# Performance work log

Hardware: AMD Instinct MI355X
Metric: run time of the kernel (lower is better)

The kernel has to match this reference:

```python
import jax, jax.numpy as jnp
import numpy as np

B, S, T = 32, 128, 64
V, E, H = 32000, 256, 512


def setup_inputs() -> dict:
    key = jax.random.key(0)
    ks = jax.random.split(key, 32)
    n = jax.random.normal

    def lin(k, fi, fo):
        kw, kb = jax.random.split(k)
        s = 1.0 / np.sqrt(fi)
        return (jax.random.uniform(kw, (fi, fo), jnp.float32, -s, s),
                jax.random.uniform(kb, (fo,), jnp.float32, -s, s))

    W_enc, b_enc = lin(ks[4], 2 * H, H)      # attention.enc_h_in
    W_prev, b_prev = lin(ks[5], H, H)        # attention.prev_s_in
    W_att, b_att = lin(ks[6], H, 1)          # attention.linear
    Wi_g, bi_g = lin(ks[7], E, 2 * H)        # cell.input_weights
    Wh_g, bh_g = lin(ks[8], H, 2 * H)        # cell.hidden_weights
    Wc_g, bc_g = lin(ks[9], 2 * H, 2 * H)    # cell.ctx_weights
    Wi, bi = lin(ks[10], E, H)               # cell.input_in
    Wh, bh = lin(ks[11], H, H)               # cell.hidden_in
    Wc, bc = lin(ks[12], 2 * H, H)           # cell.ctx_in
    W_out, b_out = lin(ks[13], H, V)         # dec2word

    return dict(
        content=n(ks[0], (B, H), jnp.float32),
        sentiment=n(ks[1], (B, H), jnp.float32),
        hiddens=n(ks[2], (B, S, 2 * H), jnp.float32),
        target=jax.random.randint(ks[3], (B, T), 0, V, jnp.int32),
        embed=n(ks[14], (V, E), jnp.float32) * 0.02,
        W_enc=W_enc, b_enc=b_enc, W_prev=W_prev, b_prev=b_prev,
        W_att=W_att, b_att=b_att,
        Wi_g=Wi_g, bi_g=bi_g, Wh_g=Wh_g, bh_g=bh_g, Wc_g=Wc_g, bc_g=bc_g,
        Wi=Wi, bi=bi, Wh=Wh, bh=bh, Wc=Wc, bc=bc,
        W_out=W_out, b_out=b_out,
    )


def reference(content, sentiment, hiddens, target, embed,
              W_enc, b_enc, W_prev, b_prev, W_att, b_att,
              Wi_g, bi_g, Wh_g, bh_g, Wc_g, bc_g,
              Wi, bi, Wh, bh, Wc, bc, W_out, b_out):
    tgt_emb = embed[target]                       # [B, T, E]
    enc_proj = hiddens @ W_enc + b_enc            # [B, S, H], timestep-invariant

    def step(prev_s, x_t):
        # additive attention
        q = prev_s @ W_prev + b_prev              # [B, H]
        h = jnp.tanh(enc_proj + q[:, None, :])    # [B, S, H]
        score = h @ W_att + b_att                 # [B, S, 1]
        alpha = jax.nn.softmax(score, axis=1)     # over source positions
        ctx = jnp.einsum('bsi,bsh->bh', alpha, hiddens)  # [B, 2H]
        # GRU-like cell (original uses only the first gate, as written)
        gates = x_t @ Wi_g + bi_g + prev_s @ Wh_g + bh_g + ctx @ Wc_g + bc_g
        reset_gate, _update_gate = jnp.split(gates, 2, axis=1)
        r = jax.nn.sigmoid(reset_gate)
        s_tilde = jnp.tanh(x_t @ Wi + bi + prev_s @ Wh + bh + ctx @ Wc + bc)
        new_s = (1.0 - r) * prev_s + r * s_tilde
        return new_s, new_s

    _, dec_h = jax.lax.scan(step, content, jnp.swapaxes(tgt_emb, 0, 1))
    dec_h = jnp.swapaxes(dec_h, 0, 1)             # [B, T, H]
    style_logits = sentiment @ W_out + b_out      # [B, V], same every step
    outputs = (dec_h @ W_out + b_out) + 0.5 * style_logits[:, None, :]
    return outputs                                # [B, T, V]
```

## Files before the change

kernel.cpp:

```cpp
#include <hip/hip_runtime.h>
#include <hip/hip_bf16.h>
#include <math.h>

#define NB 32
#define NS 128
#define NT 64
#define NV 32000
#define NE 256
#define NH 512

typedef short s16x8 __attribute__((ext_vector_type(8)));
typedef float f32x4 __attribute__((ext_vector_type(4)));

__device__ __forceinline__ unsigned short f2bf(float x) {
    union { float f; unsigned u; } v; v.f = x;
    unsigned r = v.u + 0x7FFFu + ((v.u >> 16) & 1u);
    return (unsigned short)(r >> 16);
}
__device__ __forceinline__ float bf2f(short h) {
    union { unsigned u; float f; } x;
    x.u = ((unsigned)(unsigned short)h) << 16;
    return x.f;
}

__device__ __forceinline__ void st_pt(unsigned long long* p, unsigned pay, unsigned tag) {
    unsigned long long v = (unsigned long long)pay | ((unsigned long long)tag << 32);
    asm volatile("global_store_dwordx2 %0, %1, off sc0 sc1" :: "v"(p), "v"(v) : "memory");
}
__device__ __forceinline__ void ld8_pt(const unsigned long long* b0, unsigned long long* v) {
    unsigned long long v0, v1, v2, v3, v4, v5, v6, v7;
    asm volatile(
        "global_load_dwordx2 %0, %8, off sc0 sc1\n\t"
        "global_load_dwordx2 %1, %9, off sc0 sc1\n\t"
        "global_load_dwordx2 %2, %10, off sc0 sc1\n\t"
        "global_load_dwordx2 %3, %11, off sc0 sc1\n\t"
        "global_load_dwordx2 %4, %12, off sc0 sc1\n\t"
        "global_load_dwordx2 %5, %13, off sc0 sc1\n\t"
        "global_load_dwordx2 %6, %14, off sc0 sc1\n\t"
        "global_load_dwordx2 %7, %15, off sc0 sc1\n\t"
        "s_waitcnt vmcnt(0)"
        : "=&v"(v0), "=&v"(v1), "=&v"(v2), "=&v"(v3),
          "=&v"(v4), "=&v"(v5), "=&v"(v6), "=&v"(v7)
        : "v"(b0), "v"(b0 + 1024), "v"(b0 + 2048), "v"(b0 + 3072),
          "v"(b0 + 4096), "v"(b0 + 5120), "v"(b0 + 6144), "v"(b0 + 7168)
        : "memory");
    v[0] = v0; v[1] = v1; v[2] = v2; v[3] = v3;
    v[4] = v4; v[5] = v5; v[6] = v6; v[7] = v7;
}
__device__ __forceinline__ void ld3_pt(const unsigned long long* p0,
                                       const unsigned long long* p1,
                                       const unsigned long long* p2,
                                       unsigned long long& a, unsigned long long& b,
                                       unsigned long long& c) {
    asm volatile(
        "global_load_dwordx2 %0, %3, off sc0 sc1\n\t"
        "global_load_dwordx2 %1, %4, off sc0 sc1\n\t"
        "global_load_dwordx2 %2, %5, off sc0 sc1\n\t"
        "s_waitcnt vmcnt(0)"
        : "=&v"(a), "=&v"(b), "=&v"(c)
        : "v"(p0), "v"(p1), "v"(p2)
        : "memory");
}

__global__ void build_wfrag_k(const float* __restrict__ Wp,
                              const float* __restrict__ Whg,
                              const float* __restrict__ Wh,
                              unsigned short* __restrict__ wfrag) {
    int blk = blockIdx.x;
    int lane = threadIdx.x;
    int ct = blk >> 4, kt = blk & 15;
    int c = ct * 16 + (lane & 15);
    int kb = kt * 32 + (lane >> 4) * 8;
    s16x8 v;
#pragma unroll
    for (int j = 0; j < 8; ++j) {
        int k = kb + j;
        float x;
        if (c < 512)       x = Wp[k * 512 + c];
        else if (c < 1024) x = Whg[k * 1024 + (c - 512)];
        else               x = Wh[k * 512 + (c - 1024)];
        v[j] = (short)f2bf(x);
    }
    ((s16x8*)wfrag)[blk * 64 + lane] = v;
}

template<int MODE>
__global__ __launch_bounds__(256, 2) void gemm_mfma(
    const float* __restrict__ Af, const unsigned short* __restrict__ Abf,
    const int* __restrict__ gidx,
    const float* __restrict__ B0, const float* __restrict__ B1, const float* __restrict__ B2,
    const float* __restrict__ e0, const float* __restrict__ e1, const float* __restrict__ e2,
    const float* __restrict__ e3, const float* __restrict__ e4, const float* __restrict__ e5,
    void* __restrict__ O0v, void* __restrict__ O1v, void* __restrict__ O2v)
{
    constexpr int M   = (MODE == 0) ? 4096 : 2048;
    constexpr int K   = (MODE == 0) ? 1024 : ((MODE == 1) ? 256 : 512);
    constexpr int LDA = (MODE == 0) ? 1024 : ((MODE == 1) ? 256 : 512);
    constexpr int MB  = M / 128;

    const int bm = blockIdx.x % MB, bn = blockIdx.x / MB;
    const int m0 = bm * 128, n0 = bn * 128;

    const float* Bp; int ldb, coff;
    if constexpr (MODE == 0) {
        int sub = n0 >> 9;
        Bp   = (sub == 0) ? B0 : (sub == 1) ? B1 : B2;
        ldb  = (sub == 1) ? 1024 : 512;
        coff = n0 & 511;
    } else if constexpr (MODE == 1) {
        if (n0 < 512) { Bp = B0; ldb = 1024; coff = n0; }
        else          { Bp = B1; ldb = 512;  coff = n0 - 512; }
    } else {
        Bp = B0; ldb = 32000; coff = n0;
    }

    __shared__ unsigned short As[128 * 40];
    __shared__ unsigned short Bs[128 * 40];

    const int tid = threadIdx.x, lane = tid & 63, w = tid >> 6;
    const int wr = w >> 1, wc = w & 1;
    const int k0f = (lane >> 4) * 8;
    const int rsel = lane & 15;

    f32x4 acc[4][4];
#pragma unroll
    for (int i = 0; i < 4; ++i)
#pragma unroll
        for (int j = 0; j < 4; ++j) { f32x4 z = {0.f, 0.f, 0.f, 0.f}; acc[i][j] = z; }

    for (int kt = 0; kt < K / 32; ++kt) {
        const int k0 = kt * 32;
        __syncthreads();
#pragma unroll
        for (int i = 0; i < 16; ++i) {
            int idx = tid + i * 256;
            int r = idx >> 5, k = idx & 31;
            unsigned short v;
            if constexpr (MODE == 2) {
                v = Abf[(size_t)(m0 + r) * LDA + k0 + k];
            } else if constexpr (MODE == 1) {
                int g = gidx[m0 + r];
                v = f2bf(Af[(size_t)g * 256 + k0 + k]);
            } else {
                v = f2bf(Af[(size_t)(m0 + r) * LDA + k0 + k]);
            }
            As[r * 40 + k] = v;
        }
#pragma unroll
        for (int i = 0; i < 16; ++i) {
            int idx = tid + i * 256;
            int k = idx >> 7, c = idx & 127;
            Bs[c * 40 + k] = f2bf(Bp[(size_t)(k0 + k) * ldb + coff + c]);
        }
        __syncthreads();

        s16x8 af[4], bf[4];
#pragma unroll
        for (int i = 0; i < 4; ++i)
            af[i] = *(const s16x8*)&As[(wr * 64 + i * 16 + rsel) * 40 + k0f];
#pragma unroll
        for (int j = 0; j < 4; ++j)
            bf[j] = *(const s16x8*)&Bs[(wc * 64 + j * 16 + rsel) * 40 + k0f];
#pragma unroll
        for (int i = 0; i < 4; ++i)
#pragma unroll
            for (int j = 0; j < 4; ++j)
                acc[i][j] = __builtin_amdgcn_mfma_f32_16x16x32_bf16(af[i], bf[j], acc[i][j], 0, 0, 0);
    }

    const int rg = (lane >> 4) * 4;
#pragma unroll
    for (int i = 0; i < 4; ++i)
#pragma unroll
        for (int j = 0; j < 4; ++j) {
            int row0 = m0 + wr * 64 + i * 16 + rg;
            int col  = n0 + wc * 64 + j * 16 + rsel;
            if constexpr (MODE == 0) {
                int sub = col >> 9;
                if (sub == 0) {
                    unsigned short* Ta = (unsigned short*)O0v;
#pragma unroll
                    for (int r = 0; r < 4; ++r)
                        Ta[(size_t)(row0 + r) * 512 + col] = f2bf(tanhf(acc[i][j][r] + e0[col]));
                } else {
                    int h = col & 511;
                    int bb = row0 >> 7, s0 = row0 & 127;
                    unsigned long long pk = 0;
#pragma unroll
                    for (int r = 0; r < 4; ++r)
                        pk |= (unsigned long long)f2bf(acc[i][j][r]) << (16 * r);
                    unsigned short* dstp = (sub == 1) ? (unsigned short*)O1v : (unsigned short*)O2v;
                    *(unsigned long long*)&dstp[(size_t)((bb * 512 + h) * 128 + s0)] = pk;
                }
            } else if constexpr (MODE == 1) {
                float* Of = (float*)O0v;
                float bias;
                if (col < 512) bias = e0[col] + e1[col] + e2[col];
                else { int h = col - 512; bias = e3[h] + e4[h] + e5[h]; }
#pragma unroll
                for (int r = 0; r < 4; ++r)
                    Of[(size_t)(row0 + r) * 1024 + col] = acc[i][j][r] + bias;
            } else {
                float* Of = (float*)O0v;
#pragma unroll
                for (int r = 0; r < 4; ++r)
                    Of[(size_t)(row0 + r) * 32000 + col] = acc[i][j][r] + 1.5f * e0[col];
            }
        }
}

__global__ __launch_bounds__(1024) void scan_df(
    const float* __restrict__ content, const float* __restrict__ sentiment,
    const float* __restrict__ b_prev,  const float* __restrict__ W_att,
    const unsigned short* __restrict__ Ta_bf,
    const unsigned short* __restrict__ hWcg_t,
    const unsigned short* __restrict__ hWc_t,
    const float* __restrict__ xgxs, const unsigned short* __restrict__ wfrag,
    unsigned long long* __restrict__ Spl, unsigned long long* __restrict__ Upl,
    unsigned short* __restrict__ dh)
{
    const int b = blockIdx.x;
    const int tid = threadIdx.x, lane = tid & 63, w = tid >> 6;

    __shared__ unsigned short W_lds[3 * 16 * 64 * 8];
    __shared__ unsigned short S_lds[32 * 536];
    __shared__ float tq[512];
    __shared__ float sc[128], al[128];
    __shared__ float cg[512], cs[512];

    {
        const s16x8* src = (const s16x8*)wfrag + (size_t)b * (3 * 16 * 64);
        s16x8* dst = (s16x8*)W_lds;
        for (int i = tid; i < 3 * 16 * 64; i += 1024) dst[i] = src[i];
    }
    float s_reg = 0.f, senth = 0.f, bprev_h = 0.f;
    if (tid < 512) {
        s_reg   = content[b * 512 + tid];
        senth   = 0.5f * sentiment[b * 512 + tid];
        bprev_h = b_prev[tid];
    }
    float wv[8];
    {
        const f32x4* wa = (const f32x4*)&W_att[lane * 8];
        f32x4 a0 = wa[0], a1 = wa[1];
#pragma unroll
        for (int j = 0; j < 4; ++j) { wv[j] = a0[j]; wv[4 + j] = a1[j]; }
    }
    const int kbase = (lane >> 4) * 8;

    if (tid < 512) {
        float nsn = __shfl_down(s_reg, 1, 64);
        if (!(lane & 1)) {
            unsigned pay = (unsigned)f2bf(s_reg) | ((unsigned)f2bf(nsn) << 16);
            st_pt(&Spl[b * 256 + (tid >> 1)], pay, 1u);
        }
    }

    for (int t = 0; t < 64; ++t) {
        const unsigned want = (unsigned)(t + 1);
        const size_t xrow = (size_t)b * 64 + t;
        float xg_pre = 0.f, xs_pre = 0.f;
        if (tid < 512) {
            xg_pre = xgxs[xrow * 1024 + tid];
            xs_pre = xgxs[xrow * 1024 + 512 + tid];
        }

        {
            unsigned long long v[8];
            const unsigned long long* base = &Spl[tid];
            ld8_pt(base, v);
            for (;;) {
                bool ok = true;
#pragma unroll
                for (int ii = 0; ii < 8; ++ii) ok &= ((unsigned)(v[ii] >> 32) == want);
                if (ok) break;
                ld8_pt(base, v);
            }
#pragma unroll
            for (int ii = 0; ii < 8; ++ii) {
                int idx = tid + ii * 1024;
                int r = idx >> 8, c = (idx & 255) * 2;
                *(unsigned*)&S_lds[r * 536 + c] = (unsigned)v[ii];
            }
        }
        __syncthreads();

        if (w < 6) {
            const int mt = w & 1, ct = w >> 1;
            const int arow = mt * 16 + (lane & 15);
            f32x4 ae = {0.f, 0.f, 0.f, 0.f}, ao = {0.f, 0.f, 0.f, 0.f};
            const s16x8* wl = (const s16x8*)W_lds;
#pragma unroll
            for (int kt = 0; kt < 16; kt += 2) {
                s16x8 a0 = *(const s16x8*)&S_lds[arow * 536 + kt * 32 + kbase];
                s16x8 a1 = *(const s16x8*)&S_lds[arow * 536 + (kt + 1) * 32 + kbase];
                ae = __builtin_amdgcn_mfma_f32_16x16x32_bf16(a0, wl[(ct * 16 + kt) * 64 + lane], ae, 0, 0, 0);
                ao = __builtin_amdgcn_mfma_f32_16x16x32_bf16(a1, wl[(ct * 16 + kt + 1) * 64 + lane], ao, 0, 0, 0);
            }
            f32x4 a4 = ae + ao;
            const int cout = b * 48 + ct * 16 + (lane & 15);
            const int rbase = mt * 16 + (lane >> 4) * 4;
#pragma unroll
            for (int r = 0; r < 4; ++r)
                st_pt(&Upl[(size_t)(rbase + r) * 1536 + cout], __float_as_uint(a4[r]), want);
        }

        float guv = 0.f, suv = 0.f;
        if (tid < 512) {
            unsigned long long u0, u1, u2;
            const unsigned long long* q0 = &Upl[b * 1536 + tid];
            const unsigned long long* q1 = &Upl[b * 1536 + 512 + tid];
            const unsigned long long* q2 = &Upl[b * 1536 + 1024 + tid];
            ld3_pt(q0, q1, q2, u0, u1, u2);
            while (((unsigned)(u0 >> 32) != want) | ((unsigned)(u1 >> 32) != want) |
                   ((unsigned)(u2 >> 32) != want)) {
                ld3_pt(q0, q1, q2, u0, u1, u2);
            }
            float qv = __uint_as_float((unsigned)u0);
            guv = __uint_as_float((unsigned)u1);
            suv = __uint_as_float((unsigned)u2);
            tq[tid] = tanhf(qv + bprev_h);
        }
        __syncthreads();

        {
            float tqv[8];
            const f32x4* tp = (const f32x4*)&tq[lane * 8];
            f32x4 t0 = tp[0], t1 = tp[1];
#pragma unroll
            for (int j = 0; j < 4; ++j) { tqv[j] = t0[j]; tqv[4 + j] = t1[j]; }
#pragma unroll
            for (int s8 = 0; s8 < 8; ++s8) {
                int s = w * 8 + s8;
                s16x8 tv = *(const s16x8*)&Ta_bf[((size_t)(b * 128 + s)) * 512 + lane * 8];
                float a = 0.f;
#pragma unroll
                for (int j = 0; j < 8; ++j) {
                    float ta = bf2f(tv[j]);
                    float num = ta + tqv[j];
                    float den = fmaf(ta, tqv[j], 1.0f);
                    a = fmaf(wv[j], num * __builtin_amdgcn_rcpf(den), a);
                }
#pragma unroll
                for (int off = 32; off; off >>= 1) a += __shfl_xor(a, off, 64);
                if (lane == 0) sc[s] = a;
            }
        }
        __syncthreads();
        if (w == 0) {
            float v0 = sc[lane], v1 = sc[lane + 64];
            float m = fmaxf(v0, v1);
#pragma unroll
            for (int off = 32; off; off >>= 1) m = fmaxf(m, __shfl_xor(m, off, 64));
            float p0 = __expf(v0 - m), p1 = __expf(v1 - m);
            float sm = p0 + p1;
#pragma unroll
            for (int off = 32; off; off >>= 1) sm += __shfl_xor(sm, off, 64);
            float inv = __builtin_amdgcn_rcpf(sm);
            al[lane] = p0 * inv; al[lane + 64] = p1 * inv;
        }
        __syncthreads();
        {
            int mat = tid >> 9, h = tid & 511;
            const s16x8* Mp = (const s16x8*)((mat ? hWc_t : hWcg_t) + ((size_t)(b * 512 + h)) * 128);
            float a0 = 0.f, a1 = 0.f;
#pragma unroll
            for (int q = 0; q < 16; ++q) {
                s16x8 v = Mp[q];
#pragma unroll
                for (int j = 0; j < 8; j += 2) {
                    a0 = fmaf(al[q * 8 + j],     bf2f(v[j]),     a0);
                    a1 = fmaf(al[q * 8 + j + 1], bf2f(v[j + 1]), a1);
                }
            }
            if (mat) cs[h] = a0 + a1; else cg[h] = a0 + a1;
        }
        __syncthreads();
        if (tid < 512) {
            int h = tid;
            float g  = guv + xg_pre + cg[h];
            float r  = __builtin_amdgcn_rcpf(1.0f + __expf(-g));
            float sp = suv + xs_pre + cs[h];
            float e  = __expf(2.0f * sp);
            float st = 1.0f - 2.0f * __builtin_amdgcn_rcpf(e + 1.0f);
            float ns = s_reg + r * (st - s_reg);
            s_reg = ns;
            dh[xrow * 512 + h] = f2bf(ns + senth);
            if (t < 63) {
                float nsn = __shfl_down(ns, 1, 64);
                if (!(lane & 1)) {
                    unsigned pay = (unsigned)f2bf(ns) | ((unsigned)f2bf(nsn) << 16);
                    st_pt(&Spl[b * 256 + (h >> 1)], pay, (unsigned)(t + 2));
                }
            }
        }
        __syncthreads();
    }
}

extern "C" void kernel_launch(void* const* d_in, const int* in_sizes, int n_in,
                              void* d_out, int out_size, void* d_ws, size_t ws_size,
                              hipStream_t stream) {
    const float* content  = (const float*)d_in[0];
    const float* sentiment= (const float*)d_in[1];
    const float* hiddens  = (const float*)d_in[2];
    const int*   target   = (const int*)  d_in[3];
    const float* embed    = (const float*)d_in[4];
    const float* W_enc = (const float*)d_in[5];  const float* b_enc = (const float*)d_in[6];
    const float* W_prev= (const float*)d_in[7];  const float* b_prev= (const float*)d_in[8];
    const float* W_att = (const float*)d_in[9];
    const float* Wi_g  = (const float*)d_in[11]; const float* bi_g  = (const float*)d_in[12];
    const float* Wh_g  = (const float*)d_in[13]; const float* bh_g  = (const float*)d_in[14];
    const float* Wc_g  = (const float*)d_in[15]; const float* bc_g  = (const float*)d_in[16];
    const float* Wi    = (const float*)d_in[17]; const float* bi    = (const float*)d_in[18];
    const float* Wh    = (const float*)d_in[19]; const float* bh    = (const float*)d_in[20];
    const float* Wc    = (const float*)d_in[21]; const float* bc    = (const float*)d_in[22];
    const float* W_out = (const float*)d_in[23]; const float* b_out = (const float*)d_in[24];
    float* out = (float*)d_out;

    char* ws = (char*)d_ws;
    unsigned short* wfrag = (unsigned short*)ws;
    unsigned long long* Spl = (unsigned long long*)(ws + 0x180000);
    unsigned long long* Upl = (unsigned long long*)(ws + 0x190000);
    unsigned short* Ta_bf   = (unsigned short*)(ws + 0x200000);
    unsigned short* hWcg_t  = (unsigned short*)(ws + 0x600000);
    unsigned short* hWc_t   = (unsigned short*)(ws + 0xA00000);
    float* xgxs     = (float*)(ws + 0xE00000);
    unsigned short* dh      = (unsigned short*)(ws + 0x1600000);

    hipMemsetAsync(ws + 0x180000, 0, 0x70000, stream);

    build_wfrag_k<<<96 * 16, 64, 0, stream>>>(W_prev, Wh_g, Wh, wfrag);

    gemm_mfma<0><<<32 * 12, 256, 0, stream>>>(
        hiddens, nullptr, nullptr, W_enc, Wc_g, Wc,
        b_enc, nullptr, nullptr, nullptr, nullptr, nullptr,
        (void*)Ta_bf, (void*)hWcg_t, (void*)hWc_t);

    gemm_mfma<1><<<16 * 8, 256, 0, stream>>>(
        embed, nullptr, target, Wi_g, Wi, nullptr,
        bi_g, bh_g, bc_g, bi, bh, bc,
        (void*)xgxs, nullptr, nullptr);

    scan_df<<<NB, 1024, 0, stream>>>(
        content, sentiment, b_prev, W_att, Ta_bf, hWcg_t, hWc_t,
        xgxs, wfrag, Spl, Upl, dh);

    gemm_mfma<2><<<16 * 250, 256, 0, stream>>>(
        nullptr, dh, nullptr, W_out, nullptr, nullptr,
        b_out, nullptr, nullptr, nullptr, nullptr, nullptr,
        (void*)out, nullptr, nullptr);

    (void)in_sizes; (void)n_in; (void)out_size; (void)ws_size;
}
```

Measured before the change: 1.369 ms.

## Halve scan block to 512 threads and keep context weights in registers

```diff
diff --git a/kernel.cpp b/kernel.cpp
--- a/kernel.cpp
+++ b/kernel.cpp
@@ -27,7 +27,8 @@
     unsigned long long v = (unsigned long long)pay | ((unsigned long long)tag << 32);
     asm volatile("global_store_dwordx2 %0, %1, off sc0 sc1" :: "v"(p), "v"(v) : "memory");
 }
-__device__ __forceinline__ void ld8_pt(const unsigned long long* b0, unsigned long long* v) {
+__device__ __forceinline__ void ld8s(const unsigned long long* p, int stride,
+                                     unsigned long long* v) {
     unsigned long long v0, v1, v2, v3, v4, v5, v6, v7;
     asm volatile(
         "global_load_dwordx2 %0, %8, off sc0 sc1\n\t"
@@ -41,8 +42,8 @@
         "s_waitcnt vmcnt(0)"
         : "=&v"(v0), "=&v"(v1), "=&v"(v2), "=&v"(v3),
           "=&v"(v4), "=&v"(v5), "=&v"(v6), "=&v"(v7)
-        : "v"(b0), "v"(b0 + 1024), "v"(b0 + 2048), "v"(b0 + 3072),
-          "v"(b0 + 4096), "v"(b0 + 5120), "v"(b0 + 6144), "v"(b0 + 7168)
+        : "v"(p), "v"(p + stride), "v"(p + 2 * stride), "v"(p + 3 * stride),
+          "v"(p + 4 * stride), "v"(p + 5 * stride), "v"(p + 6 * stride), "v"(p + 7 * stride)
         : "memory");
     v[0] = v0; v[1] = v1; v[2] = v2; v[3] = v3;
     v[4] = v4; v[5] = v5; v[6] = v6; v[7] = v7;
@@ -209,7 +210,7 @@
         }
 }
 
-__global__ __launch_bounds__(1024) void scan_df(
+__global__ __launch_bounds__(512, 1) void scan_df(
     const float* __restrict__ content, const float* __restrict__ sentiment,
     const float* __restrict__ b_prev,  const float* __restrict__ W_att,
     const unsigned short* __restrict__ Ta_bf,
@@ -221,24 +222,21 @@
 {
     const int b = blockIdx.x;
     const int tid = threadIdx.x, lane = tid & 63, w = tid >> 6;
+    const int h = tid;
 
     __shared__ unsigned short W_lds[3 * 16 * 64 * 8];
     __shared__ unsigned short S_lds[32 * 536];
     __shared__ float tq[512];
     __shared__ float sc[128], al[128];
-    __shared__ float cg[512], cs[512];
 
     {
         const s16x8* src = (const s16x8*)wfrag + (size_t)b * (3 * 16 * 64);
         s16x8* dst = (s16x8*)W_lds;
-        for (int i = tid; i < 3 * 16 * 64; i += 1024) dst[i] = src[i];
-    }
-    float s_reg = 0.f, senth = 0.f, bprev_h = 0.f;
-    if (tid < 512) {
-        s_reg   = content[b * 512 + tid];
-        senth   = 0.5f * sentiment[b * 512 + tid];
-        bprev_h = b_prev[tid];
-    }
+        for (int i = tid; i < 3 * 16 * 64; i += 512) dst[i] = src[i];
+    }
+    float s_reg   = content[b * 512 + h];
+    float senth   = 0.5f * sentiment[b * 512 + h];
+    float bprev_h = b_prev[h];
     float wv[8];
     {
         const f32x4* wa = (const f32x4*)&W_att[lane * 8];
@@ -246,39 +244,45 @@
 #pragma unroll
         for (int j = 0; j < 4; ++j) { wv[j] = a0[j]; wv[4 + j] = a1[j]; }
     }
+    s16x8 hwg[16], hws[16];
+    {
+        const s16x8* pg = (const s16x8*)&hWcg_t[((size_t)(b * 512 + h)) * 128];
+        const s16x8* ps = (const s16x8*)&hWc_t [((size_t)(b * 512 + h)) * 128];
+#pragma unroll
+        for (int q = 0; q < 16; ++q) hwg[q] = pg[q];
+#pragma unroll
+        for (int q = 0; q < 16; ++q) hws[q] = ps[q];
+    }
     const int kbase = (lane >> 4) * 8;
 
-    if (tid < 512) {
+    {
         float nsn = __shfl_down(s_reg, 1, 64);
         if (!(lane & 1)) {
             unsigned pay = (unsigned)f2bf(s_reg) | ((unsigned)f2bf(nsn) << 16);
-            st_pt(&Spl[b * 256 + (tid >> 1)], pay, 1u);
+            st_pt(&Spl[b * 256 + (h >> 1)], pay, 1u);
         }
     }
 
     for (int t = 0; t < 64; ++t) {
         const unsigned want = (unsigned)(t + 1);
         const size_t xrow = (size_t)b * 64 + t;
-        float xg_pre = 0.f, xs_pre = 0.f;
-        if (tid < 512) {
-            xg_pre = xgxs[xrow * 1024 + tid];
-            xs_pre = xgxs[xrow * 1024 + 512 + tid];
-        }
+        float xg_pre = xgxs[xrow * 1024 + h];
+        float xs_pre = xgxs[xrow * 1024 + 512 + h];
 
         {
-            unsigned long long v[8];
+            unsigned long long v[16];
             const unsigned long long* base = &Spl[tid];
-            ld8_pt(base, v);
             for (;;) {
+                ld8s(base, 512, v);
+                ld8s(base + 8 * 512, 512, v + 8);
                 bool ok = true;
 #pragma unroll
-                for (int ii = 0; ii < 8; ++ii) ok &= ((unsigned)(v[ii] >> 32) == want);
+                for (int ii = 0; ii < 16; ++ii) ok &= ((unsigned)(v[ii] >> 32) == want);
                 if (ok) break;
-                ld8_pt(base, v);
-            }
-#pragma unroll
-            for (int ii = 0; ii < 8; ++ii) {
-                int idx = tid + ii * 1024;
+            }
+#pragma unroll
+            for (int ii = 0; ii < 16; ++ii) {
+                int idx = tid + ii * 512;
                 int r = idx >> 8, c = (idx & 255) * 2;
                 *(unsigned*)&S_lds[r * 536 + c] = (unsigned)v[ii];
             }
@@ -305,12 +309,12 @@
                 st_pt(&Upl[(size_t)(rbase + r) * 1536 + cout], __float_as_uint(a4[r]), want);
         }
 
-        float guv = 0.f, suv = 0.f;
-        if (tid < 512) {
+        float guv, suv;
+        {
             unsigned long long u0, u1, u2;
-            const unsigned long long* q0 = &Upl[b * 1536 + tid];
-            const unsigned long long* q1 = &Upl[b * 1536 + 512 + tid];
-            const unsigned long long* q2 = &Upl[b * 1536 + 1024 + tid];
+            const unsigned long long* q0 = &Upl[b * 1536 + h];
+            const unsigned long long* q1 = &Upl[b * 1536 + 512 + h];
+            const unsigned long long* q2 = &Upl[b * 1536 + 1024 + h];
             ld3_pt(q0, q1, q2, u0, u1, u2);
             while (((unsigned)(u0 >> 32) != want) | ((unsigned)(u1 >> 32) != want) |
                    ((unsigned)(u2 >> 32) != want)) {
@@ -319,7 +323,7 @@
             float qv = __uint_as_float((unsigned)u0);
             guv = __uint_as_float((unsigned)u1);
             suv = __uint_as_float((unsigned)u2);
-            tq[tid] = tanhf(qv + bprev_h);
+            tq[h] = tanhf(qv + bprev_h);
         }
         __syncthreads();
 
@@ -330,8 +334,8 @@
 #pragma unroll
             for (int j = 0; j < 4; ++j) { tqv[j] = t0[j]; tqv[4 + j] = t1[j]; }
 #pragma unroll
-            for (int s8 = 0; s8 < 8; ++s8) {
-                int s = w * 8 + s8;
+            for (int i = 0; i < 16; ++i) {
+                int s = w * 16 + i;
                 s16x8 tv = *(const s16x8*)&Ta_bf[((size_t)(b * 128 + s)) * 512 + lane * 8];
                 float a = 0.f;
 #pragma unroll
@@ -347,6 +351,7 @@
             }
         }
         __syncthreads();
+
         if (w == 0) {
             float v0 = sc[lane], v1 = sc[lane + 64];
             float m = fmaxf(v0, v1);
@@ -360,27 +365,22 @@
             al[lane] = p0 * inv; al[lane + 64] = p1 * inv;
         }
         __syncthreads();
+
+        float cgv = 0.f, csv = 0.f;
+#pragma unroll
+        for (int q = 0; q < 16; ++q) {
+#pragma unroll
+            for (int j = 0; j < 8; ++j) {
+                float av = al[q * 8 + j];
+                cgv = fmaf(av, bf2f(hwg[q][j]), cgv);
+                csv = fmaf(av, bf2f(hws[q][j]), csv);
+            }
+        }
+
         {
-            int mat = tid >> 9, h = tid & 511;
-            const s16x8* Mp = (const s16x8*)((mat ? hWc_t : hWcg_t) + ((size_t)(b * 512 + h)) * 128);
-            float a0 = 0.f, a1 = 0.f;
-#pragma unroll
-            for (int q = 0; q < 16; ++q) {
-                s16x8 v = Mp[q];
-#pragma unroll
-                for (int j = 0; j < 8; j += 2) {
-                    a0 = fmaf(al[q * 8 + j],     bf2f(v[j]),     a0);
-                    a1 = fmaf(al[q * 8 + j + 1], bf2f(v[j + 1]), a1);
-                }
-            }
-            if (mat) cs[h] = a0 + a1; else cg[h] = a0 + a1;
-        }
-        __syncthreads();
-        if (tid < 512) {
-            int h = tid;
-            float g  = guv + xg_pre + cg[h];
+            float g  = guv + xg_pre + cgv;
             float r  = __builtin_amdgcn_rcpf(1.0f + __expf(-g));
-            float sp = suv + xs_pre + cs[h];
+            float sp = suv + xs_pre + csv;
             float e  = __expf(2.0f * sp);
             float st = 1.0f - 2.0f * __builtin_amdgcn_rcpf(e + 1.0f);
             float ns = s_reg + r * (st - s_reg);
@@ -442,7 +442,7 @@
         bi_g, bh_g, bc_g, bi, bh, bc,
         (void*)xgxs, nullptr, nullptr);
 
-    scan_df<<<NB, 1024, 0, stream>>>(
+    scan_df<<<NB, 512, 0, stream>>>(
         content, sentiment, b_prev, W_att, Ta_bf, hWcg_t, hWc_t,
         xgxs, wfrag, Spl, Upl, dh);
 
```

Result: slower. 1.979 ms (+44.6%).
